# Optimization experiments

Measured on AMD Instinct MI355X. Metric: run time of the kernel, lower is better.

Reference implementation:

```python
import jax, jax.numpy as jnp
import numpy as np
import math

N = 100000
E = 1600000
D_IN = 128
H = 128
OUT = 10
NEG = -1e30


def setup_inputs() -> dict:
    key = jax.random.key(0)
    ks = jax.random.split(key, 24)
    def lin(k, fi, fo):
        s = 1.0 / np.sqrt(fi)
        return jax.random.uniform(k, (fi, fo), jnp.float32, -s, s)
    inp = {
        'x': jax.random.normal(ks[0], (N, D_IN), jnp.float32),
        'edge_index': jax.random.randint(ks[1], (2, E), 0, N, jnp.int64),
        'W1': lin(ks[2], D_IN, H), 'b1': jnp.zeros((H,), jnp.float32),
        'ws1': lin(ks[3], H, 1), 'bs1': jnp.zeros((1,), jnp.float32),
        'W2': lin(ks[4], H, H), 'b2': jnp.zeros((H,), jnp.float32),
        'ws2': lin(ks[5], H, 1), 'bs2': jnp.zeros((1,), jnp.float32),
        'W3': lin(ks[6], H, H), 'b3': jnp.zeros((H,), jnp.float32),
        'ws3': lin(ks[7], H, 1), 'bs3': jnp.zeros((1,), jnp.float32),
        'M1': lin(ks[8], 2 * H, H), 'bm1': jnp.zeros((H,), jnp.float32),
        'M2': lin(ks[9], H, H // 2), 'bm2': jnp.zeros((H // 2,), jnp.float32),
        'M3': lin(ks[10], H // 2, OUT), 'bm3': jnp.zeros((OUT,), jnp.float32),
    }
    return inp


def _gcn(x, W, b, src, dst, node_mask, edge_mask):
    # GCNConv with self-loops: deg[i] = self_loop + in_degree over valid edges
    deg = node_mask + jax.ops.segment_sum(edge_mask, dst, num_segments=N)
    dinv = jnp.where(deg > 0, jax.lax.rsqrt(deg), 0.0)
    coef = edge_mask * dinv[src] * dinv[dst]            # [E]
    agg = jax.ops.segment_sum(coef[:, None] * x[src], dst, num_segments=N)
    agg = agg + (node_mask * dinv * dinv)[:, None] * x   # self-loop term
    return (agg @ W + b) * node_mask[:, None]


def _sag_pool(x, ws, bs, src, dst, node_mask, edge_mask, k):
    # score via 1-dim GCNConv, top-k (ratio 0.5) select, tanh gating, edge filtering
    score = _gcn(x, ws, bs, src, dst, node_mask, edge_mask)[:, 0]
    _, idx = jax.lax.top_k(jnp.where(node_mask > 0, score, -jnp.inf), k)
    new_mask = jnp.zeros((N,), x.dtype).at[idx].set(1.0)
    x_new = x * jnp.tanh(score)[:, None] * new_mask[:, None]
    e_new = edge_mask * new_mask[src] * new_mask[dst]
    return x_new, new_mask, e_new


def _readout(x, mask, k):
    mean = jnp.sum(x * mask[:, None], axis=0) / k
    mx = jnp.max(jnp.where(mask[:, None] > 0, x, NEG), axis=0)
    return jnp.concatenate([mean, mx])[None, :]   # [1, 2H]


def reference(x, edge_index, W1, b1, ws1, bs1, W2, b2, ws2, bs2, W3, b3, ws3, bs3, M1, bm1, M2, bm2, M3, bm3):
    src, dst = edge_index[0], edge_index[1]
    nm0 = jnp.ones((N,), jnp.float32)
    em0 = jnp.ones((E,), jnp.float32)
    k1 = math.ceil(0.5 * N)
    k2 = math.ceil(0.5 * k1)
    k3 = math.ceil(0.5 * k2)

    h1 = jax.nn.relu(_gcn(x, W1, b1, src, dst, nm0, em0))
    x1, nm1, em1 = _sag_pool(h1, ws1, bs1, src, dst, nm0, em0, k1)
    r1 = _readout(x1, nm1, k1)

    h2 = jax.nn.relu(_gcn(x1, W2, b2, src, dst, nm1, em1))
    x2, nm2, em2 = _sag_pool(h2, ws2, bs2, src, dst, nm1, em1, k2)
    r2 = _readout(x2, nm2, k2)

    h3 = jax.nn.relu(_gcn(x2, W3, b3, src, dst, nm2, em2))
    x3, nm3, em3 = _sag_pool(h3, ws3, bs3, src, dst, nm2, em2, k3)
    r3 = _readout(x3, nm3, k3)

    readout = r1 + r2 + r3                              # [1, 2H]
    y = jax.nn.relu(readout @ M1 + bm1)
    y = jax.nn.relu(y @ M2 + bm2)
    y = y @ M3 + bm3
    return jax.nn.log_softmax(y, axis=1)
```

## Files before the change

kernel.cpp:

```cpp
#include <hip/hip_runtime.h>
#include <cstdint>
#include <cstddef>

#define NN 100000
#define EE 1600000
#define HH 128
#define NB_N 391
#define NBKT 391
#define CAP 5120


typedef float f32x2 __attribute__((ext_vector_type(2)));

static __device__ __forceinline__ unsigned fsort_(float f){
  unsigned u = __float_as_uint(f);
  return (u & 0x80000000u) ? ~u : (u | 0x80000000u);
}
static __device__ __forceinline__ unsigned bfbits_(float f){
  unsigned u = __float_as_uint(f);
  return (u + 0x7FFFu + ((u >> 16) & 1u)) >> 16;
}
static __device__ __forceinline__ unsigned bfpack_(float f0, float f1){
  return bfbits_(f0) | (bfbits_(f1) << 16);
}
static __device__ __forceinline__ float bflo_(unsigned u){ return __uint_as_float(u << 16); }
static __device__ __forceinline__ float bfhi_(unsigned u){ return __uint_as_float(u & 0xFFFF0000u); }

__global__ void k_edgeflag(const int* __restrict__ ei, unsigned* __restrict__ state,
                           unsigned* __restrict__ bktcnt){
  int t = threadIdx.x;
  if(t < 64){
    int v = ei[2*t + 1];
    unsigned long long m = __ballot(v != 0);
    if(t == 0) state[8] = (m == 0ull) ? 1u : 0u;
  }
  if(t >= 12 && t < 24) state[t] = 0u;
  for(int j=t; j<NBKT; j+=256) bktcnt[j] = 0u;
}

__global__ __launch_bounds__(256) void k_binA(const int* __restrict__ ei,
                     const unsigned* __restrict__ state,
                     unsigned* __restrict__ bktcnt, unsigned* __restrict__ staging){
  __shared__ unsigned lcnt[NBKT];
  __shared__ unsigned lloc[NBKT];
  int t = threadIdx.x;
  for(int j=t; j<NBKT; j+=256){ lcnt[j] = 0u; lloc[j] = 0u; }
  bool i64 = (state[8] != 0u);
  int e0 = blockIdx.x*4096;
  int es[16], ed[16];
  #pragma unroll
  for(int k=0;k<16;k++){
    int e = e0 + k*256 + t;
    int s = -1, d = 0;
    if(e < EE){
      if(i64){ s = ei[2*e]; d = ei[2*EE + 2*e]; }
      else   { s = ei[e];   d = ei[EE + e]; }
    }
    es[k] = s; ed[k] = d;
  }
  __syncthreads();
  #pragma unroll
  for(int k=0;k<16;k++){
    if(es[k] >= 0) atomicAdd(&lcnt[ed[k]>>8], 1u);
  }
  __syncthreads();
  for(int j=t; j<NBKT; j+=256){
    unsigned c = lcnt[j];
    lcnt[j] = c ? atomicAdd(&bktcnt[j], c) : 0u;
  }
  __syncthreads();
  #pragma unroll
  for(int k=0;k<16;k++){
    if(es[k] >= 0){
      int b = ed[k] >> 8;
      unsigned off = lcnt[b] + atomicAdd(&lloc[b], 1u);
      if(off < CAP)
        staging[(unsigned)b*CAP + off] = (unsigned)es[k] | (((unsigned)(ed[k] & 255)) << 17);
    }
  }
}

__global__ __launch_bounds__(256) void k_binB(const unsigned* __restrict__ staging,
                     const unsigned* __restrict__ bktcnt,
                     int* __restrict__ rs, int* __restrict__ rl, int* __restrict__ col,
                     float* __restrict__ dinv){
  __shared__ unsigned hist[256];
  __shared__ unsigned pref[256];
  __shared__ unsigned lfill[256];
  __shared__ unsigned baseSh;
  int t = threadIdx.x;
  int b = blockIdx.x;
  unsigned s = 0;
  for(int j=t; j<b; j+=256) s += bktcnt[j];
  pref[t] = s;
  __syncthreads();
  for(int off=128; off>0; off>>=1){
    if(t < off) pref[t] += pref[t+off];
    __syncthreads();
  }
  if(t == 0) baseSh = pref[0];
  __syncthreads();
  unsigned base = baseSh;
  unsigned cnt = bktcnt[b]; if(cnt > CAP) cnt = CAP;
  hist[t] = 0u; lfill[t] = 0u;
  __syncthreads();
  const unsigned* st = staging + (unsigned)b*CAP;
  for(unsigned i=t; i<cnt; i+=256) atomicAdd(&hist[st[i]>>17], 1u);
  __syncthreads();
  unsigned h = hist[t];
  pref[t] = h;
  __syncthreads();
  for(int off=1; off<256; off<<=1){
    unsigned u = (t >= off) ? pref[t-off] : 0u;
    __syncthreads();
    pref[t] += u;
    __syncthreads();
  }
  unsigned excl = pref[t] - h;
  int node = b*256 + t;
  if(node < NN){
    rs[node] = (int)(base + excl);
    rl[node] = (int)h;
    dinv[node] = rsqrtf(1.f + (float)h);
  }
  __syncthreads();
  pref[t] = excl;
  __syncthreads();
  for(unsigned i=t; i<cnt; i+=256){
    unsigned w = st[i];
    unsigned dl = w >> 17;
    unsigned pos = base + pref[dl] + atomicAdd(&lfill[dl], 1u);
    col[pos] = (int)(w & 0x1FFFFu);
  }
}

template<int MODE>
__global__ __launch_bounds__(256) void k_gemm(const void* __restrict__ xin_,
        const float* __restrict__ gate, const float* __restrict__ dinv,
        const int* __restrict__ alist, int nrows,
        const float* __restrict__ W, unsigned short* __restrict__ y16){
  __shared__ float sX[16][68];
  __shared__ float sW[16][64];
  __shared__ int rowid[64];
  __shared__ float rowg[64];
  int row0 = blockIdx.x*64, col0 = blockIdx.y*64;
  int t = threadIdx.x;
  if(t < 64){
    int gr = row0 + t;
    int node = -1; float sc = 0.f;
    if(gr < nrows){
      node = MODE ? alist[gr] : gr;
      sc = MODE ? dinv[node]*gate[node] : dinv[node];
    }
    rowid[t] = node; rowg[t] = sc;
  }
  __syncthreads();
  int tx = t & 15, ty = t >> 4;
  float acc[4][4] = {{0.f}};
  const float* xf = (const float*)xin_;
  const unsigned short* xh = (const unsigned short*)xin_;
  for(int kb=0; kb<HH; kb+=16){
    #pragma unroll
    for(int j=0;j<4;j++){
      int r = (t>>4) + j*16;
      int k = t & 15;
      int node = rowid[r];
      float v = 0.f;
      if(node >= 0){
        if(MODE) v = __uint_as_float(((unsigned)xh[(size_t)node*HH + kb + k]) << 16);
        else     v = xf[(size_t)node*HH + kb + k];
      }
      sX[k][r] = v;
    }
    #pragma unroll
    for(int j=0;j<4;j++){
      int k = (t>>6) + j*4;
      int c = t & 63;
      sW[k][c] = W[(size_t)(kb+k)*HH + col0 + c];
    }
    __syncthreads();
    #pragma unroll
    for(int k=0;k<16;k++){
      float4 xv = *(const float4*)&sX[k][ty*4];
      float4 wv = *(const float4*)&sW[k][tx*4];
      float xs[4] = {xv.x, xv.y, xv.z, xv.w};
      float wsv[4] = {wv.x, wv.y, wv.z, wv.w};
      #pragma unroll
      for(int a=0;a<4;a++)
        #pragma unroll
        for(int b=0;b<4;b++)
          acc[a][b] += xs[a]*wsv[b];
    }
    __syncthreads();
  }
  #pragma unroll
  for(int a=0;a<4;a++){
    int r = ty*4 + a;
    int node = rowid[r];
    if(node >= 0){
      float s = rowg[r];
      uint2 o;
      o.x = bfpack_(s*acc[a][0], s*acc[a][1]);
      o.y = bfpack_(s*acc[a][2], s*acc[a][3]);
      *(uint2*)&y16[(size_t)node*HH + col0 + tx*4] = o;
    }
  }
}

#define ACCQ(V) do{ \
  f32x2 t0,t1,t2,t3; \
  t0.x=__uint_as_float((V).x<<16); t0.y=__uint_as_float((V).x&0xFFFF0000u); \
  t1.x=__uint_as_float((V).y<<16); t1.y=__uint_as_float((V).y&0xFFFF0000u); \
  t2.x=__uint_as_float((V).z<<16); t2.y=__uint_as_float((V).z&0xFFFF0000u); \
  t3.x=__uint_as_float((V).w<<16); t3.y=__uint_as_float((V).w&0xFFFF0000u); \
  a01+=t0; a23+=t1; a45+=t2; a67+=t3; }while(0)

template<int LIST>
__global__ __launch_bounds__(256) void k_agg(const unsigned short* __restrict__ y16,
        const float* __restrict__ dinv,
        const int* __restrict__ rs, const int* __restrict__ rl,
        const int* __restrict__ col, const int* __restrict__ alist,
        const float* __restrict__ bias, const float* __restrict__ wsc,
        unsigned short* __restrict__ h16, float* __restrict__ p,
        unsigned* __restrict__ hist){
  if(blockIdx.x < 512) hist[blockIdx.x*256 + threadIdx.x] = 0u;
  int w = (blockIdx.x*256 + threadIdx.x) >> 6;
  int lane = threadIdx.x & 63;
  int g = lane >> 4, c = lane & 15;
  int node = LIST ? alist[w] : w;
  float di = dinv[node];
  int e0 = rs[node], len = rl[node];
  const char* yb = (const char*)y16;
  unsigned lc16 = (unsigned)(c << 4);
  int chunk = (len + 3) >> 2;
  int ib = g*chunk;
  int ie = ib + chunk; if(ie > len) ie = len;
  f32x2 a01 = {0.f,0.f}, a23 = {0.f,0.f}, a45 = {0.f,0.f}, a67 = {0.f,0.f};
  const int* ce = col + e0;
  int i = ib;
  for(; i+3 < ie; i += 4){
    int c0 = ce[i], c1 = ce[i+1], c2 = ce[i+2], c3 = ce[i+3];
    uint4 v0 = *(const uint4*)(yb + (((unsigned)c0<<8) | lc16));
    uint4 v1 = *(const uint4*)(yb + (((unsigned)c1<<8) | lc16));
    uint4 v2 = *(const uint4*)(yb + (((unsigned)c2<<8) | lc16));
    uint4 v3 = *(const uint4*)(yb + (((unsigned)c3<<8) | lc16));
    ACCQ(v0); ACCQ(v1); ACCQ(v2); ACCQ(v3);
  }
  for(; i < ie; i++){
    int c0 = ce[i];
    uint4 v0 = *(const uint4*)(yb + (((unsigned)c0<<8) | lc16));
    ACCQ(v0);
  }
  float a0=a01.x, a1=a01.y, a2=a23.x, a3=a23.y, a4=a45.x, a5=a45.y, a6=a67.x, a7=a67.y;
  a0 += __shfl_xor(a0,16,64); a0 += __shfl_xor(a0,32,64);
  a1 += __shfl_xor(a1,16,64); a1 += __shfl_xor(a1,32,64);
  a2 += __shfl_xor(a2,16,64); a2 += __shfl_xor(a2,32,64);
  a3 += __shfl_xor(a3,16,64); a3 += __shfl_xor(a3,32,64);
  a4 += __shfl_xor(a4,16,64); a4 += __shfl_xor(a4,32,64);
  a5 += __shfl_xor(a5,16,64); a5 += __shfl_xor(a5,32,64);
  a6 += __shfl_xor(a6,16,64); a6 += __shfl_xor(a6,32,64);
  a7 += __shfl_xor(a7,16,64); a7 += __shfl_xor(a7,32,64);
  uint4 sv = *(const uint4*)(yb + (((unsigned)node<<8) | lc16));
  const float4* b4 = (const float4*)bias;
  float4 bb0 = b4[2*c], bb1 = b4[2*c+1];
  float o0 = fmaxf(fmaf(di, a0 + bflo_(sv.x), bb0.x), 0.f);
  float o1 = fmaxf(fmaf(di, a1 + bfhi_(sv.x), bb0.y), 0.f);
  float o2 = fmaxf(fmaf(di, a2 + bflo_(sv.y), bb0.z), 0.f);
  float o3 = fmaxf(fmaf(di, a3 + bfhi_(sv.y), bb0.w), 0.f);
  float o4 = fmaxf(fmaf(di, a4 + bflo_(sv.z), bb1.x), 0.f);
  float o5 = fmaxf(fmaf(di, a5 + bfhi_(sv.z), bb1.y), 0.f);
  float o6 = fmaxf(fmaf(di, a6 + bflo_(sv.w), bb1.z), 0.f);
  float o7 = fmaxf(fmaf(di, a7 + bfhi_(sv.w), bb1.w), 0.f);
  if(g == 0){
    uint4 o;
    o.x = bfpack_(o0,o1); o.y = bfpack_(o2,o3);
    o.z = bfpack_(o4,o5); o.w = bfpack_(o6,o7);
    ((uint4*)(h16 + (size_t)node*HH))[c] = o;
  }
  const float4* w4 = (const float4*)wsc;
  float4 w0 = w4[2*c], w1 = w4[2*c+1];
  float pp = o0*w0.x + o1*w0.y + o2*w0.z + o3*w0.w
           + o4*w1.x + o5*w1.y + o6*w1.z + o7*w1.w;
  pp += __shfl_xor(pp, 1, 64);
  pp += __shfl_xor(pp, 2, 64);
  pp += __shfl_xor(pp, 4, 64);
  pp += __shfl_xor(pp, 8, 64);
  if(lane == 0) p[node] = di*pp;
}

template<int LIST>
__global__ void k_score(const float* __restrict__ p, const float* __restrict__ dinv,
                        const int* __restrict__ rs, const int* __restrict__ rl,
                        const int* __restrict__ col, const int* __restrict__ alist, int n,
                        const float* __restrict__ bs, float* __restrict__ score,
                        unsigned* __restrict__ key, unsigned* __restrict__ hist){
  int w = blockIdx.x*256 + threadIdx.x;
  if(w >= n) return;
  int i = LIST ? alist[w] : w;
  float di = dinv[i];
  float s = 0.f;
  int e0 = rs[i], len = rl[i];
  const int* ce = col + e0;
  int e = 0;
  for(; e+3 < len; e += 4){
    int c0 = ce[e], c1 = ce[e+1], c2 = ce[e+2], c3 = ce[e+3];
    s += (p[c0] + p[c1]) + (p[c2] + p[c3]);
  }
  for(; e < len; e++) s += p[ce[e]];
  float sc = di*(s + p[i]) + bs[0];
  score[i] = sc;
  unsigned kv = fsort_(sc);
  key[i] = kv;
  atomicAdd(&hist[kv>>16], 1u);
}

__global__ void k_hist_lo(const unsigned* __restrict__ key, const unsigned* __restrict__ state,
                          unsigned* __restrict__ histB){
  int i = blockIdx.x*256 + threadIdx.x;
  if(i < NN){
    unsigned kv = key[i];
    if((kv >> 16) == state[0]) atomicAdd(&histB[kv & 0xFFFFu], 1u);
  }
}
__global__ void k_pick(const unsigned* __restrict__ hist, unsigned* __restrict__ state,
                       int k_in, int mode){
  __shared__ unsigned csum[256];
  int t = threadIdx.x;
  const uint4* h4 = (const uint4*)(hist + t*256);
  unsigned s = 0;
  for(int j=0;j<64;j++){ uint4 v = h4[j]; s += v.x+v.y+v.z+v.w; }
  csum[t] = s;
  __syncthreads();
  for(int off=1; off<256; off<<=1){
    unsigned v = (t+off < 256) ? csum[t+off] : 0u;
    __syncthreads();
    csum[t] += v;
    __syncthreads();
  }
  unsigned k = (mode == 0) ? (unsigned)k_in : state[1];
  unsigned above = csum[t] - s;
  if(above < k && above + s >= k){
    unsigned run = above;
    for(int j=255; j>=0; j--){
      unsigned c = hist[t*256+j];
      if(run + c >= k){
        if(mode == 0){ state[0] = (unsigned)(t*256+j); state[1] = k - run; }
        else { state[2] = (state[0] << 16) | (unsigned)(t*256+j); state[3] = k - run; }
        break;
      }
      run += c;
    }
  }
}

__global__ __launch_bounds__(256) void k_maskCR(unsigned* __restrict__ key,
        const float* __restrict__ score, const unsigned* __restrict__ state,
        const unsigned short* __restrict__ h16,
        unsigned char* __restrict__ selm, float* __restrict__ gate,
        int* __restrict__ alist_out, unsigned* __restrict__ acounter,
        float* __restrict__ rpart, int slotbase){
  __shared__ int wcnt[4];
  __shared__ int priorSh;
  __shared__ int redi[256];
  __shared__ float gl[256];
  __shared__ unsigned char slf[256];
  __shared__ float4 red[256];
  __shared__ float out2[256];
  int t = threadIdx.x;
  int i = blockIdx.x*256 + t;
  unsigned T = state[2];
  int trem = (int)state[3];
  unsigned kv = (i < NN) ? key[i] : 0u;
  bool match = (kv == T);
  unsigned long long m = __ballot(match);
  int lane = t & 63, wid = t >> 6;
  if(lane == 0) wcnt[wid] = __popcll(m);
  if(t == 0) priorSh = 0;
  __syncthreads();
  int hasMatch = wcnt[0] | wcnt[1] | wcnt[2] | wcnt[3];
  int bbase = blockIdx.x*256;
  if(hasMatch){
    int cm = 0;
    for(int j = t*4; j < bbase; j += 1024){
      uint4 kk = *(const uint4*)&key[j];
      cm += (kk.x==T) + (kk.y==T) + (kk.z==T) + (kk.w==T);
    }
    redi[t] = cm;
    __syncthreads();
    for(int off=128; off>0; off>>=1){
      if(t < off) redi[t] += redi[t+off];
      __syncthreads();
    }
    if(t == 0) priorSh = redi[0];
    __syncthreads();
  }
  int pre = 0;
  for(int w=0; w<wid; w++) pre += wcnt[w];
  int lrank = __popcll(m & ((1ull << lane) - 1ull));
  int rank = priorSh + pre + lrank;
  bool sel = (kv > T) || (match && rank < trem);
  float gg = sel ? tanhf(score[i]) : 0.f;
  gl[t] = gg;
  slf[t] = sel ? 1 : 0;
  if(i < NN){
    selm[i] = sel ? 1 : 0;
    gate[i] = gg;
    if(!sel) key[i] = 0u;
  }
  unsigned long long sm = __ballot(sel);
  unsigned abase = 0;
  if(lane == 0) abase = atomicAdd(acounter, (unsigned)__popcll(sm));
  abase = (unsigned)__shfl((int)abase, 0, 64);
  if(sel) alist_out[abase + __popcll(sm & ((1ull << lane) - 1ull))] = i;
  __syncthreads();
  int ch = t & 15;
  int slot = t >> 4;
  float mm[8] = {0,0,0,0,0,0,0,0};
  float MM[8] = {-1e30f,-1e30f,-1e30f,-1e30f,-1e30f,-1e30f,-1e30f,-1e30f};
  for(int itr=0; itr<16; itr++){
    int nl = slot + itr*16;
    int node = bbase + nl;
    if(node < NN && slf[nl]){
      float g = gl[nl];
      uint4 v = ((const uint4*)(h16 + (size_t)node*HH))[ch];
      float x0 = g*bflo_(v.x), x1 = g*bfhi_(v.x);
      float x2 = g*bflo_(v.y), x3 = g*bfhi_(v.y);
      float x4 = g*bflo_(v.z), x5 = g*bfhi_(v.z);
      float x6 = g*bflo_(v.w), x7 = g*bfhi_(v.w);
      mm[0]+=x0; mm[1]+=x1; mm[2]+=x2; mm[3]+=x3;
      mm[4]+=x4; mm[5]+=x5; mm[6]+=x6; mm[7]+=x7;
      MM[0]=fmaxf(MM[0],x0); MM[1]=fmaxf(MM[1],x1); MM[2]=fmaxf(MM[2],x2); MM[3]=fmaxf(MM[3],x3);
      MM[4]=fmaxf(MM[4],x4); MM[5]=fmaxf(MM[5],x5); MM[6]=fmaxf(MM[6],x6); MM[7]=fmaxf(MM[7],x7);
    }
  }
  #pragma unroll
  for(int half=0; half<2; half++){
    red[t] = make_float4(mm[half*4+0],mm[half*4+1],mm[half*4+2],mm[half*4+3]);
    __syncthreads();
    if(t < 16){
      float4 sacc = red[t];
      for(int j=1;j<16;j++){
        float4 o = red[t + 16*j];
        sacc.x += o.x; sacc.y += o.y; sacc.z += o.z; sacc.w += o.w;
      }
      int d = t*8 + half*4;
      out2[d+0] = sacc.x; out2[d+1] = sacc.y; out2[d+2] = sacc.z; out2[d+3] = sacc.w;
    }
    __syncthreads();
    red[t] = make_float4(MM[half*4+0],MM[half*4+1],MM[half*4+2],MM[half*4+3]);
    __syncthreads();
    if(t < 16){
      float4 sacc = red[t];
      for(int j=1;j<16;j++){
        float4 o = red[t + 16*j];
        sacc.x = fmaxf(sacc.x,o.x); sacc.y = fmaxf(sacc.y,o.y);
        sacc.z = fmaxf(sacc.z,o.z); sacc.w = fmaxf(sacc.w,o.w);
      }
      int d = 128 + t*8 + half*4;
      out2[d+0] = sacc.x; out2[d+1] = sacc.y; out2[d+2] = sacc.z; out2[d+3] = sacc.w;
    }
    __syncthreads();
  }
  rpart[(size_t)(slotbase + blockIdx.x)*256 + t] = out2[t];
}

__global__ __launch_bounds__(256) void k_compact(const int* __restrict__ alist, int n,
        const unsigned char* __restrict__ selm,
        const int* __restrict__ rs_old, const int* __restrict__ rl_old,
        const int* __restrict__ col_old,
        int* __restrict__ rs_new, int* __restrict__ rl_new, int* __restrict__ col_new,
        float* __restrict__ dinv, unsigned* __restrict__ ecnt){
  __shared__ unsigned gcnt[16];
  __shared__ unsigned gbase[16];
  __shared__ unsigned blkbase;
  int t = threadIdx.x;
  int g = t >> 4, lane = t & 15;
  int gsh = ((t >> 4) & 3) * 16;
  int idx = blockIdx.x*16 + g;
  int node = -1, e0 = 0, len = 0;
  if(idx < n){ node = alist[idx]; e0 = rs_old[node]; len = rl_old[node]; }
  int cnt = 0;
  for(int i=lane; i<len; i+=16) cnt += selm[col_old[e0+i]];
  cnt += __shfl_xor(cnt,1,64); cnt += __shfl_xor(cnt,2,64);
  cnt += __shfl_xor(cnt,4,64); cnt += __shfl_xor(cnt,8,64);
  if(lane == 0) gcnt[g] = (node >= 0) ? (unsigned)cnt : 0u;
  __syncthreads();
  if(t == 0){
    unsigned s = 0;
    for(int j=0;j<16;j++){ gbase[j] = s; s += gcnt[j]; }
    blkbase = s ? atomicAdd(ecnt, s) : 0u;
  }
  __syncthreads();
  unsigned base = blkbase + gbase[g];
  if(node >= 0 && lane == 0){
    rs_new[node] = (int)base;
    rl_new[node] = cnt;
    dinv[node] = rsqrtf(1.f + (float)cnt);
  }
  int pos = (int)base;
  for(int i0=0; i0<len; i0+=16){
    int i = i0 + lane;
    bool keep = false; int s = 0;
    if(i < len){ s = col_old[e0+i]; keep = (selm[s] != 0); }
    unsigned long long b = __ballot(keep);
    unsigned gb = (unsigned)((b >> gsh) & 0xFFFFull);
    int rank = __popc(gb & ((1u << lane) - 1u));
    if(keep) col_new[pos + rank] = s;
    pos += __popc(gb);
  }
}

__global__ void k_mlp(const float* __restrict__ rpart,
                      const float* __restrict__ M1, const float* __restrict__ bm1,
                      const float* __restrict__ M2, const float* __restrict__ bm2,
                      const float* __restrict__ M3, const float* __restrict__ bm3,
                      float* __restrict__ out){
  __shared__ float R[256];
  __shared__ float y1[128];
  __shared__ float y2[64];
  __shared__ float y3[16];
  int t = threadIdx.x;
  const float kinv[3] = {1.f/50000.f, 1.f/25000.f, 1.f/12500.f};
  if(t < 128){
    float acc = 0.f;
    for(int l=0; l<3; l++){
      float s0=0.f,s1=0.f,s2=0.f,s3=0.f;
      int base = l*NB_N;
      int j = 0;
      for(; j+3 < NB_N; j += 4){
        s0 += rpart[(size_t)(base+j  )*256 + t];
        s1 += rpart[(size_t)(base+j+1)*256 + t];
        s2 += rpart[(size_t)(base+j+2)*256 + t];
        s3 += rpart[(size_t)(base+j+3)*256 + t];
      }
      for(; j < NB_N; j++) s0 += rpart[(size_t)(base+j)*256 + t];
      acc += ((s0+s1)+(s2+s3)) * kinv[l];
    }
    R[t] = acc;
  } else {
    float acc = 0.f;
    for(int l=0; l<3; l++){
      float m0=-1e30f,m1=-1e30f,m2=-1e30f,m3=-1e30f;
      int base = l*NB_N;
      int j = 0;
      for(; j+3 < NB_N; j += 4){
        m0 = fmaxf(m0, rpart[(size_t)(base+j  )*256 + t]);
        m1 = fmaxf(m1, rpart[(size_t)(base+j+1)*256 + t]);
        m2 = fmaxf(m2, rpart[(size_t)(base+j+2)*256 + t]);
        m3 = fmaxf(m3, rpart[(size_t)(base+j+3)*256 + t]);
      }
      for(; j < NB_N; j++) m0 = fmaxf(m0, rpart[(size_t)(base+j)*256 + t]);
      acc += fmaxf(fmaxf(m0,m1), fmaxf(m2,m3));
    }
    R[t] = acc;
  }
  __syncthreads();
  if(t < 128){
    float a = bm1[t];
    for(int d=0; d<256; d++) a += R[d]*M1[d*128+t];
    y1[t] = fmaxf(a, 0.f);
  }
  __syncthreads();
  if(t < 64){
    float a = bm2[t];
    for(int d=0; d<128; d++) a += y1[d]*M2[d*64+t];
    y2[t] = fmaxf(a, 0.f);
  }
  __syncthreads();
  if(t < 10){
    float a = bm3[t];
    for(int d=0; d<64; d++) a += y2[d]*M3[d*10+t];
    y3[t] = a;
  }
  __syncthreads();
  if(t == 0){
    float mx = -1e30f;
    for(int o=0;o<10;o++) mx = fmaxf(mx, y3[o]);
    float s = 0.f;
    for(int o=0;o<10;o++) s += expf(y3[o]-mx);
    float ls = logf(s);
    for(int o=0;o<10;o++) out[o] = y3[o] - mx - ls;
  }
}

extern "C" void kernel_launch(void* const* d_in, const int* in_sizes, int n_in,
                              void* d_out, int out_size, void* d_ws, size_t ws_size,
                              hipStream_t stream){
  (void)in_sizes; (void)n_in; (void)out_size; (void)ws_size;
  const float* x  = (const float*)d_in[0];
  const int*   ei = (const int*)d_in[1];
  const float* W[3]   = {(const float*)d_in[2],  (const float*)d_in[6],  (const float*)d_in[10]};
  const float* bb[3]  = {(const float*)d_in[3],  (const float*)d_in[7],  (const float*)d_in[11]};
  const float* wsc[3] = {(const float*)d_in[4],  (const float*)d_in[8],  (const float*)d_in[12]};
  const float* bsc[3] = {(const float*)d_in[5],  (const float*)d_in[9],  (const float*)d_in[13]};
  const float* M1  = (const float*)d_in[14];
  const float* bm1 = (const float*)d_in[15];
  const float* M2  = (const float*)d_in[16];
  const float* bm2 = (const float*)d_in[17];
  const float* M3  = (const float*)d_in[18];
  const float* bm3 = (const float*)d_in[19];
  float* out = (float*)d_out;

  char* base = (char*)d_ws;
  size_t off = 0;
  auto alloc = [&](size_t bytes)->char*{
    char* ptr = base + off;
    off += (bytes + 511) & ~(size_t)511;
    return ptr;
  };
  unsigned short* y16  = (unsigned short*)alloc((size_t)NN*HH*2);
  unsigned short* h16  = (unsigned short*)alloc((size_t)NN*HH*2);
  int*      col0      = (int*)     alloc((size_t)EE*4);
  int*      col1      = (int*)     alloc((size_t)EE*4);
  int*      col2      = (int*)     alloc((size_t)EE*4);
  unsigned* staging   = (unsigned*)alloc((size_t)NBKT*CAP*4);
  int*      rs0       = (int*)     alloc((size_t)NN*4);
  int*      rl0       = (int*)     alloc((size_t)NN*4);
  int*      rs1       = (int*)     alloc((size_t)NN*4);
  int*      rl1       = (int*)     alloc((size_t)NN*4);
  int*      rs2       = (int*)     alloc((size_t)NN*4);
  int*      rl2       = (int*)     alloc((size_t)NN*4);
  float*    dinv      = (float*)   alloc((size_t)NN*4);
  float*    pbuf      = (float*)   alloc((size_t)NN*4);
  float*    score     = (float*)   alloc((size_t)NN*4);
  float*    gate      = (float*)   alloc((size_t)NN*4);
  unsigned* key       = (unsigned*)alloc((size_t)NN*4);
  unsigned char* selm = (unsigned char*)alloc((size_t)NN);
  int*      alistA    = (int*)     alloc((size_t)50000*4);
  int*      alistB    = (int*)     alloc((size_t)25000*4);
  unsigned* hist      = (unsigned*)alloc((size_t)2*65536*4);
  unsigned* bktcnt    = (unsigned*)alloc((size_t)(NBKT+1)*4);
  unsigned* state     = (unsigned*)alloc(256);
  float*    rpart     = (float*)   alloc((size_t)3*NB_N*256*4);

  k_edgeflag<<<1,256,0,stream>>>(ei, state, bktcnt);
  k_binA<<<NBKT,256,0,stream>>>(ei, state, bktcnt, staging);
  k_binB<<<NBKT,256,0,stream>>>(staging, bktcnt, rs0, rl0, col0, dinv);

  k_gemm<0><<<dim3(1563,2),256,0,stream>>>(x, nullptr, dinv, nullptr, NN, W[0], y16);
  k_agg<0><<<25000,256,0,stream>>>(y16, dinv, rs0, rl0, col0, nullptr, bb[0], wsc[0], h16, pbuf, hist);
  k_score<0><<<NB_N,256,0,stream>>>(pbuf, dinv, rs0, rl0, col0, nullptr, NN, bsc[0], score, key, hist);
  k_pick<<<1,256,0,stream>>>(hist, state, 50000, 0);
  k_hist_lo<<<NB_N,256,0,stream>>>(key, state, hist + 65536);
  k_pick<<<1,256,0,stream>>>(hist + 65536, state, 0, 1);
  k_maskCR<<<NB_N,256,0,stream>>>(key, score, state, h16, selm, gate, alistA, state+12, rpart, 0);
  k_compact<<<3125,256,0,stream>>>(alistA, 50000, selm, rs0, rl0, col0, rs1, rl1, col1, dinv, state+16);

  k_gemm<1><<<dim3(782,2),256,0,stream>>>(h16, gate, dinv, alistA, 50000, W[1], y16);
  k_agg<1><<<12500,256,0,stream>>>(y16, dinv, rs1, rl1, col1, alistA, bb[1], wsc[1], h16, pbuf, hist);
  k_score<1><<<196,256,0,stream>>>(pbuf, dinv, rs1, rl1, col1, alistA, 50000, bsc[1], score, key, hist);
  k_pick<<<1,256,0,stream>>>(hist, state, 25000, 0);
  k_hist_lo<<<NB_N,256,0,stream>>>(key, state, hist + 65536);
  k_pick<<<1,256,0,stream>>>(hist + 65536, state, 0, 1);
  k_maskCR<<<NB_N,256,0,stream>>>(key, score, state, h16, selm, gate, alistB, state+13, rpart, NB_N);
  k_compact<<<1563,256,0,stream>>>(alistB, 25000, selm, rs1, rl1, col1, rs2, rl2, col2, dinv, state+17);

  k_gemm<1><<<dim3(391,2),256,0,stream>>>(h16, gate, dinv, alistB, 25000, W[2], y16);
  k_agg<1><<<6250,256,0,stream>>>(y16, dinv, rs2, rl2, col2, alistB, bb[2], wsc[2], h16, pbuf, hist);
  k_score<1><<<98,256,0,stream>>>(pbuf, dinv, rs2, rl2, col2, alistB, 25000, bsc[2], score, key, hist);
  k_pick<<<1,256,0,stream>>>(hist, state, 12500, 0);
  k_hist_lo<<<NB_N,256,0,stream>>>(key, state, hist + 65536);
  k_pick<<<1,256,0,stream>>>(hist + 65536, state, 0, 1);
  k_maskCR<<<NB_N,256,0,stream>>>(key, score, state, h16, selm, gate, alistA, state+14, rpart, 2*NB_N);

  k_mlp<<<1,256,0,stream>>>(rpart, M1, bm1, M2, bm2, M3, bm3, out);
}
```

Measured before the change: 782.9 us.

## Use split-bf16 MFMA for node GEMMs and bitpacked selection mask

Replaces the FP32 SIMT tiled GEMM with an MFMA 16x16x32 bf16 kernel. Weights are pre-split into hi/lo bf16 parts, transposed and stored in swizzled LDS, and the split-product terms are accumulated to keep close to FP32 accuracy. The selection mask becomes a per-wavefront ballot bitmask instead of a byte array, which shrinks the random lookups in compaction. The cost is a weight-prep kernel, 64KB of LDS per block (lower occupancy), and a small accuracy change from dropping the lo*lo term.

```diff
diff --git a/kernel.cpp b/kernel.cpp
--- a/kernel.cpp
+++ b/kernel.cpp
@@ -11,6 +11,8 @@
 
 
 typedef float f32x2 __attribute__((ext_vector_type(2)));
+typedef float f32x4 __attribute__((ext_vector_type(4)));
+typedef short bf16x8 __attribute__((ext_vector_type(8)));
 
 static __device__ __forceinline__ unsigned fsort_(float f){
   unsigned u = __float_as_uint(f);
@@ -36,6 +38,25 @@
   }
   if(t >= 12 && t < 24) state[t] = 0u;
   for(int j=t; j<NBKT; j+=256) bktcnt[j] = 0u;
+}
+
+__global__ void k_wprep(const float* __restrict__ W0, const float* __restrict__ W1,
+                        const float* __restrict__ W2,
+                        unsigned short* __restrict__ WtH, unsigned short* __restrict__ WtL){
+  int m = blockIdx.x;
+  const float* W = (m==0)?W0:((m==1)?W1:W2);
+  unsigned short* th = WtH + m*16384;
+  unsigned short* tl = WtL + m*16384;
+  int t = threadIdx.x;
+  for(int i=t; i<16384; i+=256){
+    int k = i & 127, n = i >> 7;
+    float w = W[k*128 + n];
+    unsigned hb = bfbits_(w);
+    float hf = __uint_as_float(hb<<16);
+    unsigned lb = bfbits_(w - hf);
+    th[n*128 + k] = (unsigned short)hb;
+    tl[n*128 + k] = (unsigned short)lb;
+  }
 }
 
 __global__ __launch_bounds__(256) void k_binA(const int* __restrict__ ei,
@@ -135,74 +156,106 @@
 }
 
 template<int MODE>
-__global__ __launch_bounds__(256) void k_gemm(const void* __restrict__ xin_,
+__global__ __launch_bounds__(256) void k_gemmM(const void* __restrict__ xin_,
         const float* __restrict__ gate, const float* __restrict__ dinv,
         const int* __restrict__ alist, int nrows,
-        const float* __restrict__ W, unsigned short* __restrict__ y16){
-  __shared__ float sX[16][68];
-  __shared__ float sW[16][64];
-  __shared__ int rowid[64];
-  __shared__ float rowg[64];
-  int row0 = blockIdx.x*64, col0 = blockIdx.y*64;
-  int t = threadIdx.x;
-  if(t < 64){
-    int gr = row0 + t;
-    int node = -1; float sc = 0.f;
+        const unsigned short* __restrict__ WtH, const unsigned short* __restrict__ WtL,
+        unsigned short* __restrict__ y16){
+  __shared__ __attribute__((aligned(16))) unsigned short sWh[128*128];
+  __shared__ __attribute__((aligned(16))) unsigned short sWl[128*128];
+  __shared__ __attribute__((aligned(16))) unsigned short sB[4][16*128];
+  int t = threadIdx.x;
+  for(int f = t; f < 2048; f += 256){
+    int colw = f >> 4, kc = f & 15;
+    uint4 vh = *(const uint4*)(WtH + colw*128 + kc*8);
+    uint4 vl = *(const uint4*)(WtL + colw*128 + kc*8);
+    int dst = colw*128 + ((kc ^ (colw & 15)) << 3);
+    *(uint4*)&sWh[dst] = vh;
+    *(uint4*)&sWl[dst] = vl;
+  }
+  int lane = t & 63, wid = t >> 6;
+  int lg = lane >> 4, lc = lane & 15;
+  int rb = blockIdx.x*64 + wid*16;
+  int arow = rb + lc;
+  int anode = 0;
+  if(arow < nrows) anode = MODE ? alist[arow] : arow;
+  bf16x8 a_h[4], a_l[4];
+  if(MODE){
+    const unsigned short* xp = (const unsigned short*)xin_ + (size_t)anode*HH + lg*8;
+    #pragma unroll
+    for(int kw=0;kw<4;kw++) a_h[kw] = *(const bf16x8*)(xp + kw*32);
+  } else {
+    const float* xp = (const float*)xin_ + (size_t)anode*HH + lg*8;
+    #pragma unroll
+    for(int kw=0;kw<4;kw++){
+      float4 x0 = *(const float4*)(xp + kw*32);
+      float4 x1 = *(const float4*)(xp + kw*32 + 4);
+      float xs[8] = {x0.x,x0.y,x0.z,x0.w,x1.x,x1.y,x1.z,x1.w};
+      #pragma unroll
+      for(int e=0;e<8;e++){
+        unsigned hb = bfbits_(xs[e]);
+        float hf = __uint_as_float(hb<<16);
+        unsigned lb = bfbits_(xs[e]-hf);
+        a_h[kw][e] = (short)hb;
+        a_l[kw][e] = (short)lb;
+      }
+    }
+  }
+  __syncthreads();
+  f32x4 acc[8];
+  #pragma unroll
+  for(int c=0;c<8;c++) acc[c] = (f32x4){0.f,0.f,0.f,0.f};
+  #pragma unroll
+  for(int kw=0;kw<4;kw++){
+    int kch = kw*4 + lg;
+    bf16x8 bh[8], bl[8];
+    #pragma unroll
+    for(int c=0;c<8;c++){
+      int idx = (c*16 + lc)*128 + ((kch ^ lc) << 3);
+      bh[c] = *(const bf16x8*)&sWh[idx];
+      bl[c] = *(const bf16x8*)&sWl[idx];
+    }
+    #pragma unroll
+    for(int c=0;c<8;c++)
+      acc[c] = __builtin_amdgcn_mfma_f32_16x16x32_bf16(a_h[kw], bh[c], acc[c], 0,0,0);
+    if(MODE){
+      #pragma unroll
+      for(int c=0;c<8;c++)
+        acc[c] = __builtin_amdgcn_mfma_f32_16x16x32_bf16(a_h[kw], bl[c], acc[c], 0,0,0);
+    } else {
+      #pragma unroll
+      for(int c=0;c<8;c++)
+        acc[c] = __builtin_amdgcn_mfma_f32_16x16x32_bf16(a_l[kw], bh[c], acc[c], 0,0,0);
+      #pragma unroll
+      for(int c=0;c<8;c++)
+        acc[c] = __builtin_amdgcn_mfma_f32_16x16x32_bf16(a_h[kw], bl[c], acc[c], 0,0,0);
+    }
+  }
+  float s[4];
+  #pragma unroll
+  for(int r=0;r<4;r++){
+    int gr = rb + lg*4 + r;
+    float sv = 0.f;
     if(gr < nrows){
-      node = MODE ? alist[gr] : gr;
-      sc = MODE ? dinv[node]*gate[node] : dinv[node];
-    }
-    rowid[t] = node; rowg[t] = sc;
-  }
-  __syncthreads();
-  int tx = t & 15, ty = t >> 4;
-  float acc[4][4] = {{0.f}};
-  const float* xf = (const float*)xin_;
-  const unsigned short* xh = (const unsigned short*)xin_;
-  for(int kb=0; kb<HH; kb+=16){
+      int nd = MODE ? alist[gr] : gr;
+      sv = MODE ? dinv[nd]*gate[nd] : dinv[nd];
+    }
+    s[r] = sv;
+  }
+  #pragma unroll
+  for(int c=0;c<8;c++){
     #pragma unroll
-    for(int j=0;j<4;j++){
-      int r = (t>>4) + j*16;
-      int k = t & 15;
-      int node = rowid[r];
-      float v = 0.f;
-      if(node >= 0){
-        if(MODE) v = __uint_as_float(((unsigned)xh[(size_t)node*HH + kb + k]) << 16);
-        else     v = xf[(size_t)node*HH + kb + k];
-      }
-      sX[k][r] = v;
-    }
-    #pragma unroll
-    for(int j=0;j<4;j++){
-      int k = (t>>6) + j*4;
-      int c = t & 63;
-      sW[k][c] = W[(size_t)(kb+k)*HH + col0 + c];
-    }
-    __syncthreads();
-    #pragma unroll
-    for(int k=0;k<16;k++){
-      float4 xv = *(const float4*)&sX[k][ty*4];
-      float4 wv = *(const float4*)&sW[k][tx*4];
-      float xs[4] = {xv.x, xv.y, xv.z, xv.w};
-      float wsv[4] = {wv.x, wv.y, wv.z, wv.w};
-      #pragma unroll
-      for(int a=0;a<4;a++)
-        #pragma unroll
-        for(int b=0;b<4;b++)
-          acc[a][b] += xs[a]*wsv[b];
-    }
-    __syncthreads();
-  }
-  #pragma unroll
-  for(int a=0;a<4;a++){
-    int r = ty*4 + a;
-    int node = rowid[r];
-    if(node >= 0){
-      float s = rowg[r];
-      uint2 o;
-      o.x = bfpack_(s*acc[a][0], s*acc[a][1]);
-      o.y = bfpack_(s*acc[a][2], s*acc[a][3]);
-      *(uint2*)&y16[(size_t)node*HH + col0 + tx*4] = o;
+    for(int r=0;r<4;r++)
+      sB[wid][(lg*4+r)*128 + c*16 + lc] = (unsigned short)bfbits_(acc[c][r]*s[r]);
+  }
+  #pragma unroll
+  for(int it=0; it<4; it++){
+    int row = it*4 + lg;
+    int grow = rb + row;
+    uint4 v = *(const uint4*)&sB[wid][row*128 + lc*8];
+    if(grow < nrows){
+      int nd = MODE ? alist[grow] : grow;
+      *(uint4*)&y16[(size_t)nd*HH + lc*8] = v;
     }
   }
 }
@@ -356,7 +409,7 @@
 __global__ __launch_bounds__(256) void k_maskCR(unsigned* __restrict__ key,
         const float* __restrict__ score, const unsigned* __restrict__ state,
         const unsigned short* __restrict__ h16,
-        unsigned char* __restrict__ selm, float* __restrict__ gate,
+        unsigned* __restrict__ selb, float* __restrict__ gate,
         int* __restrict__ alist_out, unsigned* __restrict__ acounter,
         float* __restrict__ rpart, int slotbase){
   __shared__ int wcnt[4];
@@ -403,11 +456,15 @@
   gl[t] = gg;
   slf[t] = sel ? 1 : 0;
   if(i < NN){
-    selm[i] = sel ? 1 : 0;
     gate[i] = gg;
     if(!sel) key[i] = 0u;
   }
   unsigned long long sm = __ballot(sel);
+  if(lane == 0){
+    int widx = blockIdx.x*4 + wid;
+    selb[widx*2]   = (unsigned)sm;
+    selb[widx*2+1] = (unsigned)(sm >> 32);
+  }
   unsigned abase = 0;
   if(lane == 0) abase = atomicAdd(acounter, (unsigned)__popcll(sm));
   abase = (unsigned)__shfl((int)abase, 0, 64);
@@ -465,7 +522,7 @@
 }
 
 __global__ __launch_bounds__(256) void k_compact(const int* __restrict__ alist, int n,
-        const unsigned char* __restrict__ selm,
+        const unsigned* __restrict__ selb,
         const int* __restrict__ rs_old, const int* __restrict__ rl_old,
         const int* __restrict__ col_old,
         int* __restrict__ rs_new, int* __restrict__ rl_new, int* __restrict__ col_new,
@@ -480,7 +537,10 @@
   int node = -1, e0 = 0, len = 0;
   if(idx < n){ node = alist[idx]; e0 = rs_old[node]; len = rl_old[node]; }
   int cnt = 0;
-  for(int i=lane; i<len; i+=16) cnt += selm[col_old[e0+i]];
+  for(int i=lane; i<len; i+=16){
+    int s = col_old[e0+i];
+    cnt += (int)((selb[s>>5] >> (s&31)) & 1u);
+  }
   cnt += __shfl_xor(cnt,1,64); cnt += __shfl_xor(cnt,2,64);
   cnt += __shfl_xor(cnt,4,64); cnt += __shfl_xor(cnt,8,64);
   if(lane == 0) gcnt[g] = (node >= 0) ? (unsigned)cnt : 0u;
@@ -501,7 +561,7 @@
   for(int i0=0; i0<len; i0+=16){
     int i = i0 + lane;
     bool keep = false; int s = 0;
-    if(i < len){ s = col_old[e0+i]; keep = (selm[s] != 0); }
+    if(i < len){ s = col_old[e0+i]; keep = ((selb[s>>5] >> (s&31)) & 1u) != 0u; }
     unsigned long long b = __ballot(keep);
     unsigned gb = (unsigned)((b >> gsh) & 0xFFFFull);
     int rank = __popc(gb & ((1u << lane) - 1u));
@@ -625,43 +685,46 @@
   float*    score     = (float*)   alloc((size_t)NN*4);
   float*    gate      = (float*)   alloc((size_t)NN*4);
   unsigned* key       = (unsigned*)alloc((size_t)NN*4);
-  unsigned char* selm = (unsigned char*)alloc((size_t)NN);
+  unsigned* selb      = (unsigned*)alloc((size_t)3200*4);
   int*      alistA    = (int*)     alloc((size_t)50000*4);
   int*      alistB    = (int*)     alloc((size_t)25000*4);
   unsigned* hist      = (unsigned*)alloc((size_t)2*65536*4);
   unsigned* bktcnt    = (unsigned*)alloc((size_t)(NBKT+1)*4);
   unsigned* state     = (unsigned*)alloc(256);
   float*    rpart     = (float*)   alloc((size_t)3*NB_N*256*4);
+  unsigned short* WtH = (unsigned short*)alloc((size_t)3*16384*2);
+  unsigned short* WtL = (unsigned short*)alloc((size_t)3*16384*2);
 
   k_edgeflag<<<1,256,0,stream>>>(ei, state, bktcnt);
+  k_wprep<<<3,256,0,stream>>>(W[0], W[1], W[2], WtH, WtL);
   k_binA<<<NBKT,256,0,stream>>>(ei, state, bktcnt, staging);
   k_binB<<<NBKT,256,0,stream>>>(staging, bktcnt, rs0, rl0, col0, dinv);
 
-  k_gemm<0><<<dim3(1563,2),256,0,stream>>>(x, nullptr, dinv, nullptr, NN, W[0], y16);
+  k_gemmM<0><<<1563,256,0,stream>>>(x, nullptr, dinv, nullptr, NN, WtH, WtL, y16);
   k_agg<0><<<25000,256,0,stream>>>(y16, dinv, rs0, rl0, col0, nullptr, bb[0], wsc[0], h16, pbuf, hist);
   k_score<0><<<NB_N,256,0,stream>>>(pbuf, dinv, rs0, rl0, col0, nullptr, NN, bsc[0], score, key, hist);
   k_pick<<<1,256,0,stream>>>(hist, state, 50000, 0);
   k_hist_lo<<<NB_N,256,0,stream>>>(key, state, hist + 65536);
   k_pick<<<1,256,0,stream>>>(hist + 65536, state, 0, 1);
-  k_maskCR<<<NB_N,256,0,stream>>>(key, score, state, h16, selm, gate, alistA, state+12, rpart, 0);
-  k_compact<<<3125,256,0,stream>>>(alistA, 50000, selm, rs0, rl0, col0, rs1, rl1, col1, dinv, state+16);
-
-  k_gemm<1><<<dim3(782,2),256,0,stream>>>(h16, gate, dinv, alistA, 50000, W[1], y16);
+  k_maskCR<<<NB_N,256,0,stream>>>(key, score, state, h16, selb, gate, alistA, state+12, rpart, 0);
+  k_compact<<<3125,256,0,stream>>>(alistA, 50000, selb, rs0, rl0, col0, rs1, rl1, col1, dinv, state+16);
+
+  k_gemmM<1><<<782,256,0,stream>>>(h16, gate, dinv, alistA, 50000, WtH+16384, WtL+16384, y16);
   k_agg<1><<<12500,256,0,stream>>>(y16, dinv, rs1, rl1, col1, alistA, bb[1], wsc[1], h16, pbuf, hist);
   k_score<1><<<196,256,0,stream>>>(pbuf, dinv, rs1, rl1, col1, alistA, 50000, bsc[1], score, key, hist);
   k_pick<<<1,256,0,stream>>>(hist, state, 25000, 0);
   k_hist_lo<<<NB_N,256,0,stream>>>(key, state, hist + 65536);
   k_pick<<<1,256,0,stream>>>(hist + 65536, state, 0, 1);
-  k_maskCR<<<NB_N,256,0,stream>>>(key, score, state, h16, selm, gate, alistB, state+13, rpart, NB_N);
-  k_compact<<<1563,256,0,stream>>>(alistB, 25000, selm, rs1, rl1, col1, rs2, rl2, col2, dinv, state+17);
-
-  k_gemm<1><<<dim3(391,2),256,0,stream>>>(h16, gate, dinv, alistB, 25000, W[2], y16);
+  k_maskCR<<<NB_N,256,0,stream>>>(key, score, state, h16, selb, gate, alistB, state+13, rpart, NB_N);
+  k_compact<<<1563,256,0,stream>>>(alistB, 25000, selb, rs1, rl1, col1, rs2, rl2, col2, dinv, state+17);
+
+  k_gemmM<1><<<391,256,0,stream>>>(h16, gate, dinv, alistB, 25000, WtH+2*16384, WtL+2*16384, y16);
   k_agg<1><<<6250,256,0,stream>>>(y16, dinv, rs2, rl2, col2, alistB, bb[2], wsc[2], h16, pbuf, hist);
   k_score<1><<<98,256,0,stream>>>(pbuf, dinv, rs2, rl2, col2, alistB, 25000, bsc[2], score, key, hist);
   k_pick<<<1,256,0,stream>>>(hist, state, 12500, 0);
   k_hist_lo<<<NB_N,256,0,stream>>>(key, state, hist + 65536);
   k_pick<<<1,256,0,stream>>>(hist + 65536, state, 0, 1);
-  k_maskCR<<<NB_N,256,0,stream>>>(key, score, state, h16, selm, gate, alistA, state+14, rpart, 2*NB_N);
+  k_maskCR<<<NB_N,256,0,stream>>>(key, score, state, h16, selb, gate, alistA, state+14, rpart, 2*NB_N);
 
   k_mlp<<<1,256,0,stream>>>(rpart, M1, bm1, M2, bm2, M3, bm3, out);
 }
```

Measured after the change: 738.8 us. 5.6% less time.
